# Kernel optimization log

Measured on AMD Instinct MI355X. Metric: run time of the kernel, lower is better.

The kernel has to match this reference:

```python
import jax, jax.numpy as jnp
import numpy as np

N, D = 1024, 256


def setup_inputs() -> dict:
    key = jax.random.key(0)
    k1, k2, k3, k4, k5 = jax.random.split(key, 5)
    s1 = 1.0 / np.sqrt(2 * D)  # fan_in of first linear
    s2 = 1.0 / np.sqrt(D)      # fan_in of second linear
    return {
        "nodes": jax.random.normal(k1, (N, D), dtype=jnp.float32),
        "W1": jax.random.normal(k2, (D, 2 * D), dtype=jnp.float32) * s1,
        "b1": jax.random.normal(k3, (D,), dtype=jnp.float32) * s1,
        "W2": jax.random.normal(k4, (1, D), dtype=jnp.float32) * s2,
        "b2": jax.random.normal(k5, (1,), dtype=jnp.float32) * s2,
    }


def reference(nodes, W1, b1, W2, b2):
    # Original: pair = cat([n_i, n_j], -1); A = sigmoid(Linear2(relu(Linear1(pair))))
    # Algebraically: Linear1(cat(n_i, n_j)) = n_i @ Wa^T + n_j @ Wb^T + b1
    d = nodes.shape[1]
    Wa, Wb = W1[:, :d], W1[:, d:]
    a = nodes @ Wa.T  # (N, D) row-side projection
    b = nodes @ Wb.T  # (N, D) col-side projection
    h = jax.nn.relu(a[:, None, :] + b[None, :, :] + b1)  # (N, N, D)
    logits = jnp.einsum("ijd,d->ij", h, W2[0]) + b2[0]   # (N, N)
    return jax.nn.sigmoid(logits)
```

## Files before the change

kernel.cpp:

```cpp
#include <hip/hip_runtime.h>
#include <math.h>

#define N_NODES 1024
#define DIM     256

__global__ __launch_bounds__(256, 2) void k1_gemm(
    const float* __restrict__ nodes, const float* __restrict__ W1,
    const float* __restrict__ b1, float* __restrict__ At, float* __restrict__ Bt)
{
    __shared__ float nt[DIM][33];
    __shared__ float wa[DIM][17];
    __shared__ float wb[DIM][17];

    const int t  = threadIdx.x;
    const int i0 = (blockIdx.x & 31) * 32;
    const int d0 = (blockIdx.x >> 5) * 16;

    {
        const int m = t & 7;
        const int s = t >> 3;
        const float* src = nodes + (i0 + s) * DIM;
        #pragma unroll
        for (int rep = 0; rep < 8; ++rep) {
            const int k = rep * 32 + m * 4;
            float4 v = *(const float4*)(src + k);
            nt[k+0][s] = v.x; nt[k+1][s] = v.y;
            nt[k+2][s] = v.z; nt[k+3][s] = v.w;
        }
    }
    {
        const int m = t & 15;
        const int s = t >> 4;
        const float* srcA = W1 + (d0 + s) * (2 * DIM);
        const float* srcB = srcA + DIM;
        #pragma unroll
        for (int rep = 0; rep < 4; ++rep) {
            const int k = rep * 64 + m * 4;
            float4 va = *(const float4*)(srcA + k);
            float4 vb = *(const float4*)(srcB + k);
            wa[k+0][s] = va.x; wa[k+1][s] = va.y;
            wa[k+2][s] = va.z; wa[k+3][s] = va.w;
            wb[k+0][s] = vb.x; wb[k+1][s] = vb.y;
            wb[k+2][s] = vb.z; wb[k+3][s] = vb.w;
        }
    }
    __syncthreads();

    const int tx = t & 15;
    const int ty = t >> 4;
    float aA0 = 0.f, aA1 = 0.f, aB0 = 0.f, aB1 = 0.f;

    #pragma unroll 8
    for (int k = 0; k < DIM; ++k) {
        float2 av = *(const float2*)&nt[k][tx * 2];
        float  wk = wa[k][ty];
        float  vk = wb[k][ty];
        aA0 += av.x * wk;  aA1 += av.y * wk;
        aB0 += av.x * vk;  aB1 += av.y * vk;
    }

    const int d = d0 + ty;
    const int i = i0 + tx * 2;
    const float bb = b1[d];
    float2 oa; oa.x = aA0 + bb; oa.y = aA1 + bb;
    float2 ob; ob.x = aB0;      ob.y = aB1;
    *(float2*)&At[d * N_NODES + i] = oa;
    *(float2*)&Bt[d * N_NODES + i] = ob;
}

__global__ __launch_bounds__(256, 2) void k2_pair(
    const float* __restrict__ At, const float* __restrict__ Bt,
    const float* __restrict__ W2, const float* __restrict__ b2,
    float* __restrict__ out)
{
    __shared__ float As[DIM][32];
    __shared__ float Bs[DIM][32];

    const int t  = threadIdx.x;
    const int i0 = (blockIdx.x & 31) * 32;
    const int j0 = (blockIdx.x >> 5) * 32;

    #pragma unroll
    for (int rep = 0; rep < 8; ++rep) {
        const int flat = rep * 256 + t;
        const int row  = flat >> 3;
        const int c4   = (flat & 7) * 4;
        *(float4*)&As[row][c4] = *(const float4*)(At + row * N_NODES + i0 + c4);
        *(float4*)&Bs[row][c4] = *(const float4*)(Bt + row * N_NODES + j0 + c4);
    }
    __syncthreads();

    const int tx = t & 15;
    const int ty = t >> 4;
    float acc00 = 0.f, acc01 = 0.f, acc10 = 0.f, acc11 = 0.f;

    #pragma unroll 8
    for (int d = 0; d < DIM; ++d) {
        const float w = W2[d];
        float2 a = *(const float2*)&As[d][ty * 2];
        float2 b = *(const float2*)&Bs[d][tx * 2];
        acc00 += fmaxf(a.x + b.x, 0.f) * w;
        acc01 += fmaxf(a.x + b.y, 0.f) * w;
        acc10 += fmaxf(a.y + b.x, 0.f) * w;
        acc11 += fmaxf(a.y + b.y, 0.f) * w;
    }

    const float bb = b2[0];
    float2 o0, o1;
    o0.x = 1.0f / (1.0f + __expf(-(acc00 + bb)));
    o0.y = 1.0f / (1.0f + __expf(-(acc01 + bb)));
    o1.x = 1.0f / (1.0f + __expf(-(acc10 + bb)));
    o1.y = 1.0f / (1.0f + __expf(-(acc11 + bb)));

    const int r = i0 + ty * 2;
    const int c = j0 + tx * 2;
    *(float2*)&out[(r    ) * N_NODES + c] = o0;
    *(float2*)&out[(r + 1) * N_NODES + c] = o1;
}

extern "C" void kernel_launch(void* const* d_in, const int* in_sizes, int n_in,
                              void* d_out, int out_size, void* d_ws, size_t ws_size,
                              hipStream_t stream) {
    const float* nodes = (const float*)d_in[0];
    const float* W1    = (const float*)d_in[1];
    const float* b1    = (const float*)d_in[2];
    const float* W2    = (const float*)d_in[3];
    const float* b2    = (const float*)d_in[4];
    float* out = (float*)d_out;

    float* At = (float*)d_ws;
    float* Bt = At + DIM * N_NODES;

    k1_gemm<<<512,  256, 0, stream>>>(nodes, W1, b1, At, Bt);
    k2_pair<<<1024, 256, 0, stream>>>(At, Bt, W2, b2, out);
}
```

Baseline: 99.53 us.

## Use packed f32x2 math and split D into halves to cut LDS and raise occupancy

Both kernels now accumulate in two-wide float vectors (fma, add and max builtins) so the compiler can emit packed FP32 instructions on CDNA. The D dimension is processed in two 128-wide chunks that are staged through LDS one after another, which halves shared memory per block. The pair kernel's launch bounds go from 2 to 4 blocks per CU to use that extra room. In the projection kernel the Wa and Wb weights are interleaved into a single f32x2 array. The trade-off is an extra pair of barriers and reloads per chunk, plus the risk that the packed ops are not emitted or that register limits tighten.

```diff
diff --git a/kernel.cpp b/kernel.cpp
--- a/kernel.cpp
+++ b/kernel.cpp
@@ -4,33 +4,25 @@
 #define N_NODES 1024
 #define DIM     256
 
+typedef float f32x2 __attribute__((ext_vector_type(2)));
+
+__device__ __forceinline__ f32x2 relu2(f32x2 x) {
+    return __builtin_elementwise_max(x, (f32x2)0.0f);
+}
+
 __global__ __launch_bounds__(256, 2) void k1_gemm(
     const float* __restrict__ nodes, const float* __restrict__ W1,
     const float* __restrict__ b1, float* __restrict__ At, float* __restrict__ Bt)
 {
-    __shared__ float nt[DIM][33];
-    __shared__ float wa[DIM][17];
-    __shared__ float wb[DIM][17];
+    __shared__ float nt[128][34];
+    __shared__ f32x2 wab[DIM][17];
 
     const int t  = threadIdx.x;
     const int i0 = (blockIdx.x & 31) * 32;
     const int d0 = (blockIdx.x >> 5) * 16;
 
     {
-        const int m = t & 7;
-        const int s = t >> 3;
-        const float* src = nodes + (i0 + s) * DIM;
-        #pragma unroll
-        for (int rep = 0; rep < 8; ++rep) {
-            const int k = rep * 32 + m * 4;
-            float4 v = *(const float4*)(src + k);
-            nt[k+0][s] = v.x; nt[k+1][s] = v.y;
-            nt[k+2][s] = v.z; nt[k+3][s] = v.w;
-        }
-    }
-    {
-        const int m = t & 15;
-        const int s = t >> 4;
+        const int m = t & 15, s = t >> 4;
         const float* srcA = W1 + (d0 + s) * (2 * DIM);
         const float* srcB = srcA + DIM;
         #pragma unroll
@@ -38,79 +30,100 @@
             const int k = rep * 64 + m * 4;
             float4 va = *(const float4*)(srcA + k);
             float4 vb = *(const float4*)(srcB + k);
-            wa[k+0][s] = va.x; wa[k+1][s] = va.y;
-            wa[k+2][s] = va.z; wa[k+3][s] = va.w;
-            wb[k+0][s] = vb.x; wb[k+1][s] = vb.y;
-            wb[k+2][s] = vb.z; wb[k+3][s] = vb.w;
+            wab[k+0][s] = f32x2{va.x, vb.x};
+            wab[k+1][s] = f32x2{va.y, vb.y};
+            wab[k+2][s] = f32x2{va.z, vb.z};
+            wab[k+3][s] = f32x2{va.w, vb.w};
         }
     }
-    __syncthreads();
 
     const int tx = t & 15;
     const int ty = t >> 4;
-    float aA0 = 0.f, aA1 = 0.f, aB0 = 0.f, aB1 = 0.f;
+    const int sm = t & 7, ss = t >> 3;
+    const float* nsrc = nodes + (i0 + ss) * DIM;
 
-    #pragma unroll 8
-    for (int k = 0; k < DIM; ++k) {
-        float2 av = *(const float2*)&nt[k][tx * 2];
-        float  wk = wa[k][ty];
-        float  vk = wb[k][ty];
-        aA0 += av.x * wk;  aA1 += av.y * wk;
-        aB0 += av.x * vk;  aB1 += av.y * vk;
+    f32x2 accA = {0.f, 0.f}, accB = {0.f, 0.f};
+
+    for (int kc = 0; kc < DIM; kc += 128) {
+        __syncthreads();
+        #pragma unroll
+        for (int rep = 0; rep < 4; ++rep) {
+            const int k = rep * 32 + sm * 4;
+            float4 v = *(const float4*)(nsrc + kc + k);
+            nt[k+0][ss] = v.x; nt[k+1][ss] = v.y;
+            nt[k+2][ss] = v.z; nt[k+3][ss] = v.w;
+        }
+        __syncthreads();
+
+        #pragma unroll 8
+        for (int k = 0; k < 128; ++k) {
+            f32x2 av = *(const f32x2*)&nt[k][tx * 2];
+            f32x2 wv = wab[kc + k][ty];
+            f32x2 waa = __builtin_shufflevector(wv, wv, 0, 0);
+            f32x2 wbb = __builtin_shufflevector(wv, wv, 1, 1);
+            accA = __builtin_elementwise_fma(av, waa, accA);
+            accB = __builtin_elementwise_fma(av, wbb, accB);
+        }
     }
 
     const int d = d0 + ty;
     const int i = i0 + tx * 2;
     const float bb = b1[d];
-    float2 oa; oa.x = aA0 + bb; oa.y = aA1 + bb;
-    float2 ob; ob.x = aB0;      ob.y = aB1;
-    *(float2*)&At[d * N_NODES + i] = oa;
-    *(float2*)&Bt[d * N_NODES + i] = ob;
+    f32x2 oa = accA + f32x2{bb, bb};
+    *(f32x2*)&At[d * N_NODES + i] = oa;
+    *(f32x2*)&Bt[d * N_NODES + i] = accB;
 }
 
-__global__ __launch_bounds__(256, 2) void k2_pair(
+__global__ __launch_bounds__(256, 4) void k2_pair(
     const float* __restrict__ At, const float* __restrict__ Bt,
     const float* __restrict__ W2, const float* __restrict__ b2,
     float* __restrict__ out)
 {
-    __shared__ float As[DIM][32];
-    __shared__ float Bs[DIM][32];
+    __shared__ float As[128][32];
+    __shared__ float Bs[128][32];
 
     const int t  = threadIdx.x;
     const int i0 = (blockIdx.x & 31) * 32;
     const int j0 = (blockIdx.x >> 5) * 32;
-
-    #pragma unroll
-    for (int rep = 0; rep < 8; ++rep) {
-        const int flat = rep * 256 + t;
-        const int row  = flat >> 3;
-        const int c4   = (flat & 7) * 4;
-        *(float4*)&As[row][c4] = *(const float4*)(At + row * N_NODES + i0 + c4);
-        *(float4*)&Bs[row][c4] = *(const float4*)(Bt + row * N_NODES + j0 + c4);
-    }
-    __syncthreads();
-
     const int tx = t & 15;
     const int ty = t >> 4;
-    float acc00 = 0.f, acc01 = 0.f, acc10 = 0.f, acc11 = 0.f;
 
-    #pragma unroll 8
-    for (int d = 0; d < DIM; ++d) {
-        const float w = W2[d];
-        float2 a = *(const float2*)&As[d][ty * 2];
-        float2 b = *(const float2*)&Bs[d][tx * 2];
-        acc00 += fmaxf(a.x + b.x, 0.f) * w;
-        acc01 += fmaxf(a.x + b.y, 0.f) * w;
-        acc10 += fmaxf(a.y + b.x, 0.f) * w;
-        acc11 += fmaxf(a.y + b.y, 0.f) * w;
+    f32x2 acc0 = {0.f, 0.f};
+    f32x2 acc1 = {0.f, 0.f};
+
+    for (int dc = 0; dc < DIM; dc += 128) {
+        __syncthreads();
+        #pragma unroll
+        for (int rep = 0; rep < 4; ++rep) {
+            const int flat = rep * 256 + t;
+            const int row  = flat >> 3;
+            const int c4   = (flat & 7) * 4;
+            *(float4*)&As[row][c4] = *(const float4*)(At + (dc+row) * N_NODES + i0 + c4);
+            *(float4*)&Bs[row][c4] = *(const float4*)(Bt + (dc+row) * N_NODES + j0 + c4);
+        }
+        __syncthreads();
+
+        #pragma unroll 8
+        for (int d = 0; d < 128; ++d) {
+            const float w = W2[dc + d];
+            f32x2 wv = {w, w};
+            f32x2 a2 = *(const f32x2*)&As[d][ty * 2];
+            f32x2 bj = *(const f32x2*)&Bs[d][tx * 2];
+            f32x2 axx = __builtin_shufflevector(a2, a2, 0, 0);
+            f32x2 ayy = __builtin_shufflevector(a2, a2, 1, 1);
+            acc0 = __builtin_elementwise_fma(relu2(axx + bj), wv, acc0);
+            acc1 = __builtin_elementwise_fma(relu2(ayy + bj), wv, acc1);
+        }
     }
 
     const float bb = b2[0];
+    f32x2 x0 = acc0 + f32x2{bb, bb};
+    f32x2 x1 = acc1 + f32x2{bb, bb};
     float2 o0, o1;
-    o0.x = 1.0f / (1.0f + __expf(-(acc00 + bb)));
-    o0.y = 1.0f / (1.0f + __expf(-(acc01 + bb)));
-    o1.x = 1.0f / (1.0f + __expf(-(acc10 + bb)));
-    o1.y = 1.0f / (1.0f + __expf(-(acc11 + bb)));
+    o0.x = 1.0f / (1.0f + __expf(-x0.x));
+    o0.y = 1.0f / (1.0f + __expf(-x0.y));
+    o1.x = 1.0f / (1.0f + __expf(-x1.x));
+    o1.y = 1.0f / (1.0f + __expf(-x1.y));
 
     const int r = i0 + ty * 2;
     const int c = j0 + tx * 2;
```

Measured after the change: 94.11 us. 5.5% less time.
